# Kernel optimization log

Hardware: AMD Instinct MI355X
Metric: run time of the kernel (lower is better)

Reference implementation:

```python
import jax, jax.numpy as jnp
import numpy as np

HEAD_DIM = 256
ROTARY_DIM = 128  # max(2, int(0.5*256) rounded down to even)
HALF_ROT = ROTARY_DIM // 2   # 64
HALF_HEAD = HEAD_DIM // 2    # 128
WAVELENGTH = 10000.0
ROPE_SCALING = 1.0
SOFT_CAP = 50.0
EPS = 1e-6
NQ = 8
NKV = 4
GROUPS = NQ // NKV
NEG_INF = -1e9


def rms_norm(x, scale):
    # keras-hub Gemma RMSNorm: fp32 compute, out = x * rsqrt(mean(x^2)+eps) * (1+scale)
    x32 = x.astype(jnp.float32)
    var = jnp.mean(jnp.square(x32), axis=-1, keepdims=True)
    y = x32 * jax.lax.rsqrt(var + EPS)
    return (y * (1.0 + scale.astype(jnp.float32))).astype(x.dtype)


def l2_norm(x):
    # Gemma4VNorm: pure L2 normalization over head_dim, no learned scale
    x32 = x.astype(jnp.float32)
    ss = jnp.sum(jnp.square(x32), axis=-1, keepdims=True)
    return (x32 * jax.lax.rsqrt(ss + EPS)).astype(x.dtype)


def apply_partial_rope(x):
    # x: [B, S, N, HEAD_DIM]. Partial proportional rotation: only the first
    # HALF_ROT elements of each HALF_HEAD half get rotated. RoPE inverse freqs
    # use denominator_dim = HEAD_DIM (not rotary_dim).
    S = x.shape[1]
    inv_freq = 1.0 / (WAVELENGTH ** (jnp.arange(0, ROTARY_DIM, 2, dtype=jnp.float32) / HEAD_DIM))  # [HALF_ROT]
    pos = jnp.arange(S, dtype=jnp.float32) / ROPE_SCALING
    freq = pos[:, None] * inv_freq[None, :]             # [S, HALF_ROT]
    cos = jnp.cos(freq)[None, :, None, :].astype(x.dtype)
    sin = jnp.sin(freq)[None, :, None, :].astype(x.dtype)
    x1 = x[..., :HALF_HEAD]
    x2 = x[..., HALF_HEAD:]
    x1r, x1n = x1[..., :HALF_ROT], x1[..., HALF_ROT:]
    x2r, x2n = x2[..., :HALF_ROT], x2[..., HALF_ROT:]
    # rotate-half form: [x1r, x2r]*cos + [-x2r, x1r]*sin
    y1r = x1r * cos - x2r * sin
    y2r = x2r * cos + x1r * sin
    return jnp.concatenate([y1r, x1n, y2r, x2n], axis=-1)


def setup_inputs() -> dict:
    key = jax.random.key(0)
    ks = jax.random.split(key, 6)
    B, S, D = 2, 2048, 2048
    x = jax.random.normal(ks[0], (B, S, D), jnp.float32)
    # causal mask [B, S, S]
    attention_mask = jnp.broadcast_to(jnp.tril(jnp.ones((S, S), bool))[None], (B, S, S))
    w_scale = 0.02
    Wq = jax.random.normal(ks[1], (NQ, D, HEAD_DIM), jnp.float32) * w_scale
    Wk = jax.random.normal(ks[2], (NKV, D, HEAD_DIM), jnp.float32) * w_scale
    Wv = jax.random.normal(ks[3], (NKV, D, HEAD_DIM), jnp.float32) * w_scale
    Wo = jax.random.normal(ks[4], (NQ, HEAD_DIM, D), jnp.float32) * w_scale
    q_scale = jnp.zeros((HEAD_DIM,), jnp.float32)
    k_scale = jnp.zeros((HEAD_DIM,), jnp.float32)
    return {"x": x, "attention_mask": attention_mask, "Wq": Wq, "Wk": Wk,
            "Wv": Wv, "Wo": Wo, "q_scale": q_scale, "k_scale": k_scale}


def reference(x, attention_mask, Wq, Wk, Wv, Wo, q_scale, k_scale):
    B, S, D = x.shape
    q = jnp.einsum('btd,ndh->btnh', x, Wq)
    q = apply_partial_rope(rms_norm(q, q_scale))
    k = jnp.einsum('bsd,kdh->bskh', x, Wk)
    k = apply_partial_rope(rms_norm(k, k_scale))
    v = l2_norm(jnp.einsum('bsd,kdh->bskh', x, Wv))
    # grouped-query attention, scaling = 1.0 (Gemma4 relies on QK norm)
    qg = q.reshape(B, S, NKV, GROUPS, HEAD_DIM)
    logits = jnp.einsum('btkgh,bskh->bkgts', qg, k)
    # logit soft cap
    logits = jnp.tanh(logits / SOFT_CAP) * SOFT_CAP
    mask = attention_mask[:, None, None, :, :]
    logits = jnp.where(mask, logits, NEG_INF)
    probs = jax.nn.softmax(logits.astype(jnp.float32), axis=-1).astype(logits.dtype)
    out = jnp.einsum('bkgts,bskh->btkgh', probs, v).reshape(B, S, NQ, HEAD_DIM)
    return jnp.einsum('btnh,nhd->btd', out, Wo)
```

## Files before the change

kernel.cpp:

```cpp
#include <hip/hip_runtime.h>

#define AS1 __attribute__((address_space(1)))
#define AS3 __attribute__((address_space(3)))

typedef __attribute__((ext_vector_type(8))) _Float16 f16x8;
typedef __attribute__((ext_vector_type(4))) float f32x4;

__device__ __forceinline__ unsigned short f2h(float f) {
    union { _Float16 h; unsigned short u; } v; v.h = (_Float16)f; return v.u;
}

__device__ __forceinline__ void gload16(const void* g, void* l) {
    __builtin_amdgcn_global_load_lds((const AS1 unsigned int*)g, (AS3 unsigned int*)l, 16, 0, 0);
}

__global__ __launch_bounds__(256) void k_cvt(const float* __restrict__ src,
                                             unsigned short* __restrict__ dst, int n4) {
    int i = blockIdx.x * 256 + threadIdx.x;
    if (i >= n4) return;
    float4 v = ((const float4*)src)[i];
    ushort4 o;
    o.x = f2h(v.x); o.y = f2h(v.y); o.z = f2h(v.z); o.w = f2h(v.w);
    ((ushort4*)dst)[i] = o;
}

__global__ __launch_bounds__(256) void k_transpose_cvt(const float* __restrict__ src,
                                                       unsigned short* __restrict__ dst,
                                                       int ld_src, int ld_dst,
                                                       long zs_src, long zs_dst) {
    __shared__ float tile[32][33];
    long sb = (long)blockIdx.z * zs_src;
    long db = (long)blockIdx.z * zs_dst;
    int c0 = blockIdx.x * 32, r0 = blockIdx.y * 32;
    int tx = threadIdx.x, ty = threadIdx.y;
#pragma unroll
    for (int i = 0; i < 4; i++)
        tile[ty + i * 8][tx] = src[sb + (long)(r0 + ty + i * 8) * ld_src + c0 + tx];
    __syncthreads();
#pragma unroll
    for (int i = 0; i < 4; i++)
        dst[db + (long)(c0 + ty + i * 8) * ld_dst + r0 + tx] = f2h(tile[tx][ty + i * 8]);
}

__global__ __launch_bounds__(256) void k_gemm_f16(const unsigned short* __restrict__ A,
                                                  const unsigned short* __restrict__ Bt,
                                                  float* __restrict__ C,
                                                  int M, int N, int K) {
    __shared__ unsigned short As[128 * 64];
    __shared__ unsigned short Bs[128 * 64];
    int tid = threadIdx.x;
    int lane = tid & 63, wid = tid >> 6;
    int g = lane >> 4, fr = lane & 15;
    int rowA0 = blockIdx.y * 128;
    int colB0 = blockIdx.x * 128;

    f32x4 zero = {0.f, 0.f, 0.f, 0.f};
    f32x4 acc[4][4];
#pragma unroll
    for (int mi = 0; mi < 4; mi++)
#pragma unroll
        for (int ni = 0; ni < 4; ni++) acc[mi][ni] = zero;

    const unsigned short* ag[4];
    const unsigned short* bg[4];
#pragma unroll
    for (int j = 0; j < 4; j++) {
        int id = j * 256 + tid;
        int r = id >> 3;
        int c = (id & 7) ^ (r & 7);
        ag[j] = A + (size_t)(rowA0 + r) * K + c * 8;
        bg[j] = Bt + (size_t)(colB0 + r) * K + c * 8;
    }

    int nK = K >> 6;
    for (int kt = 0; kt < nK; kt++) {
#pragma unroll
        for (int j = 0; j < 4; j++) {
            int id = j * 256 + tid;
            gload16(ag[j], As + id * 8);
            gload16(bg[j], Bs + id * 8);
            ag[j] += 64; bg[j] += 64;
        }
        __syncthreads();
#pragma unroll
        for (int kk = 0; kk < 2; kk++) {
            f16x8 af[4], bfr[4];
#pragma unroll
            for (int mi = 0; mi < 4; mi++) {
                int r = (wid >> 1) * 64 + mi * 16 + fr;
                af[mi] = *(const f16x8*)(As + r * 64 + ((((kk << 2) + g) ^ (r & 7)) << 3));
            }
#pragma unroll
            for (int ni = 0; ni < 4; ni++) {
                int r = (wid & 1) * 64 + ni * 16 + fr;
                bfr[ni] = *(const f16x8*)(Bs + r * 64 + ((((kk << 2) + g) ^ (r & 7)) << 3));
            }
#pragma unroll
            for (int mi = 0; mi < 4; mi++)
#pragma unroll
                for (int ni = 0; ni < 4; ni++)
                    acc[mi][ni] = __builtin_amdgcn_mfma_f32_16x16x32_f16(af[mi], bfr[ni], acc[mi][ni], 0, 0, 0);
        }
        __syncthreads();
    }

#pragma unroll
    for (int mi = 0; mi < 4; mi++) {
        int row = rowA0 + (wid >> 1) * 64 + mi * 16 + g * 4;
#pragma unroll
        for (int ni = 0; ni < 4; ni++) {
            int col = colB0 + (wid & 1) * 64 + ni * 16 + fr;
#pragma unroll
            for (int r = 0; r < 4; r++)
                C[(size_t)(row + r) * N + col] = acc[mi][ni][r];
        }
    }
}

__global__ __launch_bounds__(256) void k_norm_rope(float* __restrict__ qkv,
                                                   const float* __restrict__ q_scale,
                                                   const float* __restrict__ k_scale,
                                                   unsigned short* __restrict__ Qh,
                                                   unsigned short* __restrict__ Kh) {
    __shared__ float Y[256];
    __shared__ float red[4];
    int blk = blockIdx.x;
    int bt = blk >> 4, slot = blk & 15;
    int b = bt >> 11, t = bt & 2047;
    int h = threadIdx.x;
    int lane = h & 63, wid = h >> 6;

    float x = qkv[(size_t)bt * 4096 + slot * 256 + h];
    float v = x * x;
#pragma unroll
    for (int m = 1; m < 64; m <<= 1) v += __shfl_xor(v, m);
    if (lane == 0) red[wid] = v;
    __syncthreads();
    float ss = red[0] + red[1] + red[2] + red[3];

    float y;
    if (slot < 12) {
        float fac = rsqrtf(ss * (1.0f / 256.0f) + 1e-6f);
        const float* sc = (slot < 8) ? q_scale : k_scale;
        y = x * fac * (1.0f + sc[h]);
    } else {
        float fac = rsqrtf(ss + 1e-6f);
        y = x * fac;
    }
    Y[h] = y;
    __syncthreads();

    if (slot < 12) {
        float out;
        int hm = h & 127;
        if (hm < 64) {
            float inv = exp2f(-(float)hm * 0.10381025296522993f);
            float fr = (float)t * inv;
            float s = sinf(fr), c = cosf(fr);
            float y1 = Y[hm], y2 = Y[128 + hm];
            out = (h < 128) ? (y1 * c - y2 * s) : (y2 * c + y1 * s);
        } else {
            out = y;
        }
        unsigned short hv = f2h(out);
        if (slot < 8)
            Qh[((size_t)(b * 8 + slot) * 2048 + t) * 256 + h] = hv;
        else
            Kh[((size_t)(b * 4 + (slot - 8)) * 2048 + t) * 256 + h] = hv;
    } else {
        qkv[(size_t)bt * 4096 + slot * 256 + h] = y;
    }
}

__global__ __launch_bounds__(512, 2) void k_attn(const unsigned short* __restrict__ Qhg,
                                                 const unsigned short* __restrict__ Khg,
                                                 const unsigned short* __restrict__ Vtg,
                                                 unsigned short* __restrict__ attn) {
    __shared__ __align__(16) char smem[140288];
    unsigned short* Ks = (unsigned short*)smem;
    unsigned short* Vs = (unsigned short*)(smem + 65536);
    unsigned short* Ps = (unsigned short*)(smem + 131072);
    float* ML = (float*)(smem + 139264);
    float* X = (float*)smem;

    int id = blockIdx.x;
    int bkv = id & 7;
    int npar = (id >> 3) & 1;
    int pair = id >> 4;
    int b = bkv >> 2, kv = bkv & 3;
    int n = kv * 2 + npar;
    int bn = b * 8 + n;

    int tid = threadIdx.x, lane = tid & 63, wid = tid >> 6;
    int g = lane >> 4, fr = lane & 15;
    int r2 = wid & 3, c2 = wid >> 2;

    const unsigned short* Kh = Khg + (size_t)bkv * 2048 * 256;
    const unsigned short* Vh = Vtg + (size_t)bkv * 256 * 2048;
    const unsigned short* Qb = Qhg + (size_t)bn * 2048 * 256;

    for (int half = 0; half < 2; half++) {
        int j = half ? 31 - pair : pair;
        int q0 = j * 64 + r2 * 16;

        const unsigned short* qrow = Qb + (size_t)(q0 + fr) * 256;
        f16x8 aq[8];
#pragma unroll
        for (int kk = 0; kk < 8; kk++) aq[kk] = *(const f16x8*)(qrow + kk * 32 + g * 8);

        f32x4 zero4 = {0.f, 0.f, 0.f, 0.f};
        f32x4 o[16];
#pragma unroll
        for (int i2 = 0; i2 < 16; i2++) o[i2] = zero4;
        float m_run[4] = {-1e30f, -1e30f, -1e30f, -1e30f};
        float l_run[4] = {0.f, 0.f, 0.f, 0.f};

        auto STAGE = [&](int bufi, int kt2) {
            int k0s = kt2 * 64;
#pragma unroll
            for (int t2 = 0; t2 < 4; t2++) {
                int c_ = t2 * 512 + tid;
                int r = c_ >> 5, c = (c_ & 31) ^ (r & 7);
                gload16(Kh + ((size_t)(k0s + r) * 256 + c * 8), Ks + bufi * 16384 + c_ * 8);
                int d = c_ >> 3, cv = (c_ & 7) ^ (d & 7);
                gload16(Vh + ((size_t)d * 2048 + k0s + cv * 8), Vs + bufi * 16384 + c_ * 8);
            }
        };

        STAGE(0, 0);
        __syncthreads();

        for (int kt = 0; kt <= j; kt++) {
            int cur = kt & 1;
            if (kt < j) STAGE(cur ^ 1, kt + 1);

            const unsigned short* KH = Ks + cur * 16384;
            const unsigned short* VC = Vs + cur * 16384;
            int k0 = kt * 64;

            f32x4 se[2] = {zero4, zero4}, so2[2] = {zero4, zero4};
            __builtin_amdgcn_s_setprio(1);
#pragma unroll
            for (int kk = 0; kk < 8; kk += 2) {
#pragma unroll
                for (int ni = 0; ni < 2; ni++) {
                    int kr = c2 * 32 + ni * 16 + fr;
                    f16x8 bk0 = *(const f16x8*)(KH + kr * 256 + (((kk << 2) + g) ^ (kr & 7)) * 8);
                    f16x8 bk1 = *(const f16x8*)(KH + kr * 256 + ((((kk + 1) << 2) + g) ^ (kr & 7)) * 8);
                    se[ni] = __builtin_amdgcn_mfma_f32_16x16x32_f16(aq[kk], bk0, se[ni], 0, 0, 0);
                    so2[ni] = __builtin_amdgcn_mfma_f32_16x16x32_f16(aq[kk + 1], bk1, so2[ni], 0, 0, 0);
                }
            }
            __builtin_amdgcn_s_setprio(0);

            float p[2][4];
#pragma unroll
            for (int ni = 0; ni < 2; ni++)
#pragma unroll
                for (int r = 0; r < 4; r++) {
                    float s = se[ni][r] + so2[ni][r];
                    float e = __expf(0.04f * s);
                    s = 50.f - 100.f * __builtin_amdgcn_rcpf(1.f + e);
                    int key = k0 + c2 * 32 + ni * 16 + fr;
                    int qr = q0 + g * 4 + r;
                    if (key > qr) s = -1e9f;
                    p[ni][r] = s;
                }

            float sw[4];
#pragma unroll
            for (int r = 0; r < 4; r++) {
                float m = fmaxf(p[0][r], p[1][r]);
#pragma unroll
                for (int sft = 1; sft < 16; sft <<= 1) m = fmaxf(m, __shfl_xor(m, sft));
                float mnew = fmaxf(m_run[r], m);
                sw[r] = __expf(m_run[r] - mnew);
                m_run[r] = mnew;
                float p0 = __expf(p[0][r] - mnew); p[0][r] = p0;
                float p1 = __expf(p[1][r] - mnew); p[1][r] = p1;
                float sum = p0 + p1;
#pragma unroll
                for (int sft = 1; sft < 16; sft <<= 1) sum += __shfl_xor(sum, sft);
                l_run[r] = l_run[r] * sw[r] + sum;
            }

            unsigned short* Pw = Ps + wid * 512;
#pragma unroll
            for (int ni = 0; ni < 2; ni++)
#pragma unroll
                for (int r = 0; r < 4; r++) {
                    int q = g * 4 + r, kl = ni * 16 + fr;
                    Pw[q * 32 + (((kl >> 3) ^ (q & 3)) << 3) + (kl & 7)] = f2h(p[ni][r]);
                }
            f16x8 ap = *(const f16x8*)(Pw + fr * 32 + ((g ^ (fr & 3)) << 3));

            __builtin_amdgcn_s_setprio(1);
#pragma unroll
            for (int nt = 0; nt < 16; nt++) {
                int dr = nt * 16 + fr;
                f16x8 bv = *(const f16x8*)(VC + dr * 64 + ((((c2 << 2) + g) ^ (dr & 7)) << 3));
                f32x4 ot = o[nt];
#pragma unroll
                for (int r = 0; r < 4; r++) ot[r] *= sw[r];
                o[nt] = __builtin_amdgcn_mfma_f32_16x16x32_f16(ap, bv, ot, 0, 0, 0);
            }
            __builtin_amdgcn_s_setprio(0);
            __syncthreads();
        }

        int mlbase = ((c2 * 4 + r2) * 4 + g) * 4;
        if (fr == 0) {
#pragma unroll
            for (int r = 0; r < 4; r++) {
                ML[(mlbase + r) * 2] = m_run[r];
                ML[(mlbase + r) * 2 + 1] = l_run[r];
            }
        }
        __syncthreads();
        int plbase = (((1 - c2) * 4 + r2) * 4 + g) * 4;
        float wS[4], linv[4];
#pragma unroll
        for (int r = 0; r < 4; r++) {
            float mp = ML[(plbase + r) * 2], lp = ML[(plbase + r) * 2 + 1];
            float ms = fmaxf(m_run[r], mp);
            wS[r] = __expf(m_run[r] - ms);
            float wp = __expf(mp - ms);
            linv[r] = __builtin_amdgcn_rcpf(l_run[r] * wS[r] + lp * wp);
        }
        float* Xl = X + (r2 * 64 + lane) * 68;
        if (c2 == 1) {
#pragma unroll
            for (int nt = 0; nt < 16; nt++)
#pragma unroll
                for (int r = 0; r < 4; r++) Xl[nt * 4 + r] = o[nt][r] * wS[r];
        }
        __syncthreads();
        if (c2 == 0) {
#pragma unroll
            for (int nt = 0; nt < 16; nt++)
#pragma unroll
                for (int r = 0; r < 4; r++) {
                    float val = (o[nt][r] * wS[r] + Xl[nt * 4 + r]) * linv[r];
                    int qr = q0 + g * 4 + r;
                    attn[(size_t)(b * 2048 + qr) * 2048 + n * 256 + nt * 16 + fr] = f2h(val);
                }
        }
        __syncthreads();
    }
}

extern "C" void kernel_launch(void* const* d_in, const int* in_sizes, int n_in,
                              void* d_out, int out_size, void* d_ws, size_t ws_size,
                              hipStream_t stream) {
    const float* x       = (const float*)d_in[0];
    const float* Wq      = (const float*)d_in[2];
    const float* Wk      = (const float*)d_in[3];
    const float* Wv      = (const float*)d_in[4];
    const float* Wo      = (const float*)d_in[5];
    const float* q_scale = (const float*)d_in[6];
    const float* k_scale = (const float*)d_in[7];
    float* out = (float*)d_out;
    char* ws = (char*)d_ws;

    const size_t MB = 1024 * 1024;
    unsigned short* xh    = (unsigned short*)ws;
    unsigned short* Qh    = (unsigned short*)ws;
    unsigned short* WT    = (unsigned short*)(ws + 16 * MB);
    unsigned short* Kh    = (unsigned short*)(ws + 16 * MB);
    unsigned short* Vt    = (unsigned short*)(ws + 24 * MB);
    unsigned short* WoT   = (unsigned short*)(ws + 32 * MB);
    float*          qkv   = (float*)(ws + 40 * MB);
    unsigned short* attnb = (unsigned short*)(ws + 40 * MB);

    dim3 tb(32, 8);
    k_cvt<<<dim3(8192), dim3(256), 0, stream>>>(x, xh, 2097152);
    k_transpose_cvt<<<dim3(8, 64, 8), tb, 0, stream>>>(Wq, WT, 256, 2048, 524288L, 524288L);
    k_transpose_cvt<<<dim3(8, 64, 4), tb, 0, stream>>>(Wk, WT + (size_t)2048 * 2048, 256, 2048, 524288L, 524288L);
    k_transpose_cvt<<<dim3(8, 64, 4), tb, 0, stream>>>(Wv, WT + (size_t)3072 * 2048, 256, 2048, 524288L, 524288L);

    k_gemm_f16<<<dim3(32, 32), dim3(256), 0, stream>>>(xh, WT, qkv, 4096, 4096, 2048);
    k_norm_rope<<<dim3(65536), dim3(256), 0, stream>>>(qkv, q_scale, k_scale, Qh, Kh);
    for (int b = 0; b < 2; b++)
        k_transpose_cvt<<<dim3(8, 64, 4), tb, 0, stream>>>(qkv + (size_t)b * 2048 * 4096 + 3072,
                                                           Vt + (size_t)b * 4 * 256 * 2048,
                                                           4096, 2048, 256L, 524288L);
    k_attn<<<dim3(256), dim3(512), 0, stream>>>(Qh, Kh, Vt, attnb);

    k_transpose_cvt<<<dim3(64, 64, 1), tb, 0, stream>>>(Wo, WoT, 2048, 2048, 0L, 0L);
    k_gemm_f16<<<dim3(16, 32), dim3(256), 0, stream>>>(attnb, WoT, out, 4096, 2048, 2048);
}
```

Baseline: 299.0 us.

## Add 256x256 pipelined QKV GEMM and lazy softmax rescaling in attention

Replaces the 128x128 QKV projection GEMM with a new 512-thread 256x256-tile kernel. It double-buffers LDS through direct global-to-LDS loads, interleaves loads with MFMA phases under explicit barriers and vmcnt waits, and remaps block IDs to group tiles. Separately, the attention kernel now rescales the running max and output accumulator only when some row's max grows by more than a threshold, and defers the cross-lane sum of the softmax denominator to after the loop. The goal is higher MFMA utilisation in the GEMM and fewer exp/multiply operations per attention step. The cost is heavy LDS use (128KB) with one block per CU, and a larger gap allowed between the stale and true max before rescaling.

```diff
diff --git a/kernel.cpp b/kernel.cpp
--- a/kernel.cpp
+++ b/kernel.cpp
@@ -13,6 +13,10 @@
 __device__ __forceinline__ void gload16(const void* g, void* l) {
     __builtin_amdgcn_global_load_lds((const AS1 unsigned int*)g, (AS3 unsigned int*)l, 16, 0, 0);
 }
+
+#define GBAR() __builtin_amdgcn_s_barrier()
+#define VM4()  asm volatile("s_waitcnt vmcnt(4)" ::: "memory")
+#define VM0()  asm volatile("s_waitcnt vmcnt(0)" ::: "memory")
 
 __global__ __launch_bounds__(256) void k_cvt(const float* __restrict__ src,
                                              unsigned short* __restrict__ dst, int n4) {
@@ -40,6 +44,143 @@
 #pragma unroll
     for (int i = 0; i < 4; i++)
         dst[db + (long)(c0 + ty + i * 8) * ld_dst + r0 + tx] = f2h(tile[tx][ty + i * 8]);
+}
+
+
+template<int BUF, int MIH>
+__device__ __forceinline__ void rdA(const unsigned short* SA, int wm, int fr, int g,
+                                    f16x8 (&af)[4][2]) {
+#pragma unroll
+    for (int m = 0; m < 4; m++)
+#pragma unroll
+        for (int kk = 0; kk < 2; kk++) {
+            int pos = wm * 64 + m * 16 + fr;
+            af[m][kk] = *(const f16x8*)(SA + BUF * 16384 + MIH * 8192 + pos * 64 +
+                                        (((kk * 4 + g) ^ (fr & 7)) << 3));
+        }
+}
+
+template<int BUF, int NIH>
+__device__ __forceinline__ void rdB(const unsigned short* SB, int wn, int fr, int g,
+                                    f16x8 (&bf)[2][2]) {
+#pragma unroll
+    for (int ni2 = 0; ni2 < 2; ni2++)
+#pragma unroll
+        for (int kk = 0; kk < 2; kk++) {
+            int pos = wn * 32 + ni2 * 16 + fr;
+            bf[ni2][kk] = *(const f16x8*)(SB + BUF * 16384 + NIH * 8192 + pos * 64 +
+                                          (((kk * 4 + g) ^ (fr & 7)) << 3));
+        }
+}
+
+template<int MIH, int NIH>
+__device__ __forceinline__ void mm16(f16x8 (&af)[4][2], f16x8 (&bf)[2][2], f32x4 (&acc)[8][4]) {
+    __builtin_amdgcn_s_setprio(1);
+#pragma unroll
+    for (int m = 0; m < 4; m++)
+#pragma unroll
+        for (int ni2 = 0; ni2 < 2; ni2++)
+#pragma unroll
+            for (int kk = 0; kk < 2; kk++)
+                acc[MIH * 4 + m][NIH * 2 + ni2] = __builtin_amdgcn_mfma_f32_16x16x32_f16(
+                    af[m][kk], bf[ni2][kk], acc[MIH * 4 + m][NIH * 2 + ni2], 0, 0, 0);
+    __builtin_amdgcn_s_setprio(0);
+}
+
+__global__ __launch_bounds__(512, 1) void k_gemm256(const unsigned short* __restrict__ A,
+                                                    const unsigned short* __restrict__ Bt,
+                                                    float* __restrict__ C,
+                                                    int M, int N, int K, int nbx) {
+    __shared__ __align__(16) unsigned short sm[65536];
+    unsigned short* SA = sm;
+    unsigned short* SB = sm + 32768;
+
+    int tid = threadIdx.x, lane = tid & 63, wid = tid >> 6;
+    int g = lane >> 4, fr = lane & 15;
+    int wm = wid >> 2, wn = wid & 3;
+
+    int bid = blockIdx.x;
+    int sid = (bid & 7) * ((int)gridDim.x >> 3) + (bid >> 3);
+    int by = sid / nbx, bx = sid % nbx;
+    int rowA0 = by * 256, colB0 = bx * 256;
+
+    f32x4 acc[8][4];
+#pragma unroll
+    for (int mi = 0; mi < 8; mi++)
+#pragma unroll
+        for (int ni = 0; ni < 4; ni++) acc[mi][ni] = (f32x4){0.f, 0.f, 0.f, 0.f};
+
+    auto stA = [&](int buf, int h, int kt) {
+#pragma unroll
+        for (int t = 0; t < 2; t++) {
+            int i = t * 512 + tid;
+            int pos = i >> 3;
+            int grow = rowA0 + ((pos >> 6) << 7) + h * 64 + (pos & 63);
+            int cg = (i & 7) ^ (pos & 7);
+            gload16(A + (size_t)grow * K + kt * 64 + cg * 8,
+                    SA + buf * 16384 + h * 8192 + pos * 64 + (i & 7) * 8);
+        }
+    };
+    auto stB = [&](int buf, int h, int kt) {
+#pragma unroll
+        for (int t = 0; t < 2; t++) {
+            int i = t * 512 + tid;
+            int pos = i >> 3;
+            int gcol = colB0 + ((pos >> 5) << 6) + h * 32 + (pos & 31);
+            int cg = (i & 7) ^ (pos & 7);
+            gload16(Bt + (size_t)gcol * K + kt * 64 + cg * 8,
+                    SB + buf * 16384 + h * 8192 + pos * 64 + (i & 7) * 8);
+        }
+    };
+
+    int nT = K >> 6;
+    stA(0, 0, 0); stB(0, 0, 0); stA(0, 1, 0); stB(0, 1, 0);
+    stA(1, 0, 1); stB(1, 0, 1);
+    VM4();
+    GBAR();
+
+    f16x8 af[4][2], bf[2][2];
+    int nIt = nT >> 1;
+    for (int it = 0; it < nIt; it++) {
+        int T = it * 2;
+        bool s36 = (T + 2 < nT), s78 = (T + 3 < nT);
+        rdA<0, 0>(SA, wm, fr, g, af); rdB<0, 0>(SB, wn, fr, g, bf);
+        stA(1, 1, T + 1);
+        GBAR(); mm16<0, 0>(af, bf, acc); GBAR();
+        rdB<0, 1>(SB, wn, fr, g, bf);
+        stB(1, 1, T + 1);
+        GBAR(); mm16<0, 1>(af, bf, acc); GBAR();
+        rdA<0, 1>(SA, wm, fr, g, af); rdB<0, 0>(SB, wn, fr, g, bf);
+        if (s36) stA(0, 0, T + 2);
+        GBAR(); mm16<1, 0>(af, bf, acc); GBAR();
+        rdB<0, 1>(SB, wn, fr, g, bf);
+        if (s36) { stB(0, 0, T + 2); VM4(); } else { VM0(); }
+        GBAR(); mm16<1, 1>(af, bf, acc); GBAR();
+        rdA<1, 0>(SA, wm, fr, g, af); rdB<1, 0>(SB, wn, fr, g, bf);
+        if (s36) stA(0, 1, T + 2);
+        GBAR(); mm16<0, 0>(af, bf, acc); GBAR();
+        rdB<1, 1>(SB, wn, fr, g, bf);
+        if (s36) stB(0, 1, T + 2);
+        GBAR(); mm16<0, 1>(af, bf, acc); GBAR();
+        rdA<1, 1>(SA, wm, fr, g, af); rdB<1, 0>(SB, wn, fr, g, bf);
+        if (s78) stA(1, 0, T + 3);
+        GBAR(); mm16<1, 0>(af, bf, acc); GBAR();
+        rdB<1, 1>(SB, wn, fr, g, bf);
+        if (s78) { stB(1, 0, T + 3); VM4(); } else { VM0(); }
+        GBAR(); mm16<1, 1>(af, bf, acc); GBAR();
+    }
+
+#pragma unroll
+    for (int mi = 0; mi < 8; mi++) {
+        int row = rowA0 + wm * 128 + mi * 16 + g * 4;
+#pragma unroll
+        for (int ni = 0; ni < 4; ni++) {
+            int col = colB0 + wn * 64 + ni * 16 + fr;
+#pragma unroll
+            for (int r = 0; r < 4; r++)
+                C[(size_t)(row + r) * N + col] = acc[mi][ni][r];
+        }
+    }
 }
 
 __global__ __launch_bounds__(256) void k_gemm_f16(const unsigned short* __restrict__ A,
@@ -267,21 +408,35 @@
                     p[ni][r] = s;
                 }
 
-            float sw[4];
+            float mrow[4];
 #pragma unroll
             for (int r = 0; r < 4; r++) {
                 float m = fmaxf(p[0][r], p[1][r]);
 #pragma unroll
                 for (int sft = 1; sft < 16; sft <<= 1) m = fmaxf(m, __shfl_xor(m, sft));
-                float mnew = fmaxf(m_run[r], m);
-                sw[r] = __expf(m_run[r] - mnew);
-                m_run[r] = mnew;
-                float p0 = __expf(p[0][r] - mnew); p[0][r] = p0;
-                float p1 = __expf(p[1][r] - mnew); p[1][r] = p1;
-                float sum = p0 + p1;
-#pragma unroll
-                for (int sft = 1; sft < 16; sft <<= 1) sum += __shfl_xor(sum, sft);
-                l_run[r] = l_run[r] * sw[r] + sum;
+                mrow[r] = m;
+            }
+            int needs = (mrow[0] > m_run[0] + 8.f) || (mrow[1] > m_run[1] + 8.f) ||
+                        (mrow[2] > m_run[2] + 8.f) || (mrow[3] > m_run[3] + 8.f);
+            if (__any(needs)) {
+                float sw[4];
+#pragma unroll
+                for (int r = 0; r < 4; r++) {
+                    float mnew = fmaxf(m_run[r], mrow[r]);
+                    sw[r] = __expf(m_run[r] - mnew);
+                    m_run[r] = mnew;
+                    l_run[r] *= sw[r];
+                }
+#pragma unroll
+                for (int nt = 0; nt < 16; nt++)
+#pragma unroll
+                    for (int r = 0; r < 4; r++) o[nt][r] *= sw[r];
+            }
+#pragma unroll
+            for (int r = 0; r < 4; r++) {
+                float p0 = __expf(p[0][r] - m_run[r]); p[0][r] = p0;
+                float p1 = __expf(p[1][r] - m_run[r]); p[1][r] = p1;
+                l_run[r] += p0 + p1;
             }
 
             unsigned short* Pw = Ps + wid * 512;
@@ -299,13 +454,18 @@
             for (int nt = 0; nt < 16; nt++) {
                 int dr = nt * 16 + fr;
                 f16x8 bv = *(const f16x8*)(VC + dr * 64 + ((((c2 << 2) + g) ^ (dr & 7)) << 3));
-                f32x4 ot = o[nt];
-#pragma unroll
-                for (int r = 0; r < 4; r++) ot[r] *= sw[r];
-                o[nt] = __builtin_amdgcn_mfma_f32_16x16x32_f16(ap, bv, ot, 0, 0, 0);
+                o[nt] = __builtin_amdgcn_mfma_f32_16x16x32_f16(ap, bv, o[nt], 0, 0, 0);
             }
             __builtin_amdgcn_s_setprio(0);
             __syncthreads();
+        }
+
+#pragma unroll
+        for (int r = 0; r < 4; r++) {
+            float l = l_run[r];
+#pragma unroll
+            for (int sft = 1; sft < 16; sft <<= 1) l += __shfl_xor(l, sft);
+            l_run[r] = l;
         }
 
         int mlbase = ((c2 * 4 + r2) * 4 + g) * 4;
@@ -378,7 +538,7 @@
     k_transpose_cvt<<<dim3(8, 64, 4), tb, 0, stream>>>(Wk, WT + (size_t)2048 * 2048, 256, 2048, 524288L, 524288L);
     k_transpose_cvt<<<dim3(8, 64, 4), tb, 0, stream>>>(Wv, WT + (size_t)3072 * 2048, 256, 2048, 524288L, 524288L);
 
-    k_gemm_f16<<<dim3(32, 32), dim3(256), 0, stream>>>(xh, WT, qkv, 4096, 4096, 2048);
+    k_gemm256<<<dim3(256), dim3(512), 0, stream>>>(xh, WT, qkv, 4096, 4096, 2048, 16);
     k_norm_rope<<<dim3(65536), dim3(256), 0, stream>>>(qkv, q_scale, k_scale, Qh, Kh);
     for (int b = 0; b < 2; b++)
         k_transpose_cvt<<<dim3(8, 64, 4), tb, 0, stream>>>(qkv + (size_t)b * 2048 * 4096 + 3072,
```

Measured after the change: 275.4 us. 1.09x faster.
